# Optimization experiments

Measured on AMD Instinct MI355X. Metric: run time of the kernel, lower is better.

The kernel has to match this reference:

```python
import jax, jax.numpy as jnp
import numpy as np

INPUT_SIZE = 256
HIDDEN_SIZE = 512
OUTPUT_SIZE = 256
SEQ_LEN = 32768


def setup_inputs() -> dict:
    key = jax.random.key(0)
    k_x, k_wx, k_wh, k_wy = jax.random.split(key, 4)
    x = jax.random.normal(k_x, (SEQ_LEN, INPUT_SIZE), dtype=jnp.float32)
    Wx = jax.random.normal(k_wx, (HIDDEN_SIZE, INPUT_SIZE), dtype=jnp.float32) * np.sqrt(2.0 / (INPUT_SIZE + HIDDEN_SIZE))
    Wh = jax.random.normal(k_wh, (HIDDEN_SIZE, HIDDEN_SIZE), dtype=jnp.float32) * np.sqrt(1.0 / HIDDEN_SIZE)
    Wy = jax.random.normal(k_wy, (OUTPUT_SIZE, HIDDEN_SIZE), dtype=jnp.float32) * np.sqrt(2.0 / (HIDDEN_SIZE + OUTPUT_SIZE))
    bh = jnp.zeros((HIDDEN_SIZE, 1), dtype=jnp.float32)
    by = jnp.zeros((OUTPUT_SIZE, 1), dtype=jnp.float32)
    return {"x": x, "Wx": Wx, "Wh": Wh, "Wy": Wy, "bh": bh, "by": by}


def reference(x, Wx, Wh, Wy, bh, by):
    # x: [T, I]; Wx: [H, I]; Wh: [H, H]; Wy: [O, H]; bh: [H,1]; by: [O,1]
    bh_v = bh[:, 0]  # [H]
    by_v = by[:, 0]  # [O]
    h0 = jnp.zeros((Wh.shape[0],), dtype=x.dtype)

    def step(h, x_t):
        # h_t = tanh(Wx @ x_t + Wh @ h_{t-1} + bh)
        h_new = jnp.tanh(Wx @ x_t + Wh @ h + bh_v)
        return h_new, h_new

    _, h_hist = jax.lax.scan(step, h0, x)  # [T, H]
    # y_t = Wy @ h_t + by, concatenated and flattened -> [T * O]
    y = h_hist @ Wy.T + by_v  # [T, O]
    return y.reshape(-1)
```

## Files before the change

### kernel.cpp

```cpp
#include <hip/hip_runtime.h>

#define SEQ 32768
#define ISZ 256
#define HSZ 512
#define OSZ 256
#define NLAUNCH 64
#define RTHREADS 576
#define SENT 0x7FAAAAAAu
#define KFAST 8
#define LATCH_T 48

typedef unsigned long long u64;
typedef _Float16 half2_t __attribute__((ext_vector_type(2)));

#if defined(__has_builtin)
#if __has_builtin(__builtin_amdgcn_fdot2)
#define HAVE_FDOT2 1
#endif
#endif

__device__ __forceinline__ float dot2f(half2_t a, half2_t b, float c) {
#ifdef HAVE_FDOT2
  return __builtin_amdgcn_fdot2(a, b, c, false);
#else
  return fmaf((float)a.x, (float)b.x, fmaf((float)a.y, (float)b.y, c));
#endif
}
__device__ __forceinline__ half2_t bch2(unsigned u) {
  return __builtin_bit_cast(half2_t, u);
}
__device__ __forceinline__ unsigned pkrtz_u(float x, float y) {
  return __builtin_bit_cast(unsigned, __builtin_amdgcn_cvt_pkrtz(x, y));
}

__global__ __launch_bounds__(256) void gemm_bt_bias(
    const float* __restrict__ A, const float* __restrict__ W,
    const float* __restrict__ bias, float* __restrict__ C,
    int M, int N, int K)
{
  __shared__ float As[32][68];
  __shared__ float Bs[32][68];
  const int tx = threadIdx.x;
  const int tn = tx & 15, tm = tx >> 4;
  const int m0 = blockIdx.x * 64, n0 = blockIdx.y * 64;
  const int kl = tx & 31;
  const int rl = tx >> 5;
  float acc[4][4] = {};

  for (int kt = 0; kt < K; kt += 32) {
#pragma unroll
    for (int i = 0; i < 8; ++i) {
      int m = rl + i * 8;
      As[kl][m] = A[(size_t)(m0 + m) * K + kt + kl];
      Bs[kl][m] = W[(size_t)(n0 + m) * K + kt + kl];
    }
    __syncthreads();
#pragma unroll
    for (int k = 0; k < 32; ++k) {
      float a[4], b[4];
#pragma unroll
      for (int i = 0; i < 4; ++i) a[i] = As[k][tm * 4 + i];
#pragma unroll
      for (int j = 0; j < 4; ++j) b[j] = Bs[k][tn * 4 + j];
#pragma unroll
      for (int i = 0; i < 4; ++i)
#pragma unroll
        for (int j = 0; j < 4; ++j)
          acc[i][j] = fmaf(a[i], b[j], acc[i][j]);
    }
    __syncthreads();
  }
#pragma unroll
  for (int i = 0; i < 4; ++i) {
    int m = m0 + tm * 4 + i;
#pragma unroll
    for (int j = 0; j < 4; ++j) {
      int n = n0 + tn * 4 + j;
      C[(size_t)m * N + n] = acc[i][j] + bias[n];
    }
  }
}

__device__ __forceinline__ float poll_sent(const float* p, unsigned sent) {
  float a, b;
  asm volatile(
      "s_waitcnt vmcnt(0)\n\t"
      "global_load_dword %0, %2, off sc0 sc1\n\t"
      "global_load_dword %1, %2, off sc0 sc1\n"
      "1:\n\t"
      "s_waitcnt vmcnt(1)\n\t"
      "v_cmp_eq_u32 vcc, %3, %0\n\t"
      "s_cbranch_vccz 3f\n\t"
      "global_load_dword %0, %2, off sc0 sc1\n\t"
      "s_waitcnt vmcnt(1)\n\t"
      "v_cmp_eq_u32 vcc, %3, %1\n\t"
      "s_cbranch_vccz 2f\n\t"
      "global_load_dword %1, %2, off sc0 sc1\n\t"
      "s_branch 1b\n"
      "2:\n\t"
      "v_mov_b32 %0, %1\n"
      "3:\n\t"
      "s_waitcnt vmcnt(0)"
      : "=&v"(a), "=&v"(b)
      : "v"(p), "v"(sent)
      : "memory", "vcc");
  return a;
}

__device__ __forceinline__ u64 load_fast(const u64* p) {
  u64 v;
  asm volatile("global_load_dwordx2 %0, %1, off sc0\n\t"
               "s_waitcnt vmcnt(0)"
               : "=v"(v) : "v"(p) : "memory");
  return v;
}
__device__ __forceinline__ void store_fast(u64* p, u64 v) {
  asm volatile("global_store_dwordx2 %0, %1, off sc0" :: "v"(p), "v"(v)
               : "memory");
}

__global__ __launch_bounds__(RTHREADS, 2) void rnn_recur(
    const float* __restrict__ P,
    const float* __restrict__ Wh,
    float* __restrict__ h_hist,
    u64* __restrict__ fring)
{
  const int b = blockIdx.x;
  if (b & 7) return;
  const int g = b >> 3;
  const int tid = threadIdx.x;
  const int w = tid >> 6;
  const int l = tid & 63;
  const int g64 = g << 6;

  __shared__ float part[2][8][64];
  __shared__ float hown[2][64];
  __shared__ int   wflag[8];
  __shared__ int   hofl;
  if (tid < 8) wflag[tid] = 0;
  if (tid == 8) hofl = 0;
  __syncthreads();

  if (w == 8) {
    float pv = P[g64 + l];
    for (int t = 0; t < SEQ; ++t) {
      const int buf = t & 1;
      int fv;
      do {
        fv = __hip_atomic_load(&wflag[l & 7], __ATOMIC_ACQUIRE,
                               __HIP_MEMORY_SCOPE_WORKGROUP);
      } while (__any((int)(fv < t + 1)));
      float s = 0.f;
#pragma unroll
      for (int q = 0; q < 8; ++q) s += part[buf][q][l];
      float xv = s + pv;
      xv = fminf(fmaxf(xv, -15.f), 15.f);
      float e = __expf(2.f * xv);
      float hn = 1.f - 2.f / (e + 1.f);
      __hip_atomic_store(&h_hist[(size_t)(t + 1) * HSZ + g64 + l], hn,
                         __ATOMIC_RELAXED, __HIP_MEMORY_SCOPE_AGENT);
      const u64 pk = ((u64)(unsigned)(t + 1) << 32) | (u64)__float_as_uint(hn);
      const int slot = (t + 1) & 3;
#pragma unroll
      for (int j = 0; j < 8; ++j)
        store_fast(fring + (((size_t)j * 4 + slot) * 8 + g) * 64 + l, pk);
      hown[(t + 1) & 1][l] = hn;
      if (l == 0)
        __hip_atomic_store(&hofl, t + 1, __ATOMIC_RELEASE,
                           __HIP_MEMORY_SCOPE_WORKGROUP);
      pv = P[(size_t)(t + 1 < SEQ ? t + 1 : SEQ - 1) * HSZ + g64 + l];
    }
    return;
  }

  const int row = g64 + l;
  const int kbase = w << 6;

  unsigned wreg[32];
  {
    const float2* ws = (const float2*)(Wh + (size_t)row * HSZ + kbase);
#pragma unroll
    for (int j = 0; j < 32; ++j) {
      float2 f = ws[j];
      unsigned u = pkrtz_u(f.x, f.y);
      asm("" : "+v"(u));
      wreg[j] = u;
    }
  }

  const bool lds_path = (w == g);
  int fastok = 0;
  int use_fast = 1;

  for (int t = 0; t < SEQ; ++t) {
    float vh = 0.f;
    if (t > 0) {
      if (lds_path) {
        while (__hip_atomic_load(&hofl, __ATOMIC_ACQUIRE,
                                 __HIP_MEMORY_SCOPE_WORKGROUP) < t) { }
        vh = hown[t & 1][l];
      } else {
        int got = 0;
        if (use_fast) {
          const u64* fp = fring + (((size_t)g * 4 + (t & 3)) * 8 + w) * 64 + l;
          for (int k = 0; k < KFAST; ++k) {
            u64 v = load_fast(fp);
            if (__all((int)((unsigned)(v >> 32) == (unsigned)t))) {
              vh = __uint_as_float((unsigned)v);
              got = 1;
              break;
            }
          }
          if (t <= LATCH_T) {
            fastok += got;
            if (t == LATCH_T && fastok < LATCH_T - 8) use_fast = 0;
          }
        }
        if (!got)
          vh = poll_sent(h_hist + (size_t)t * HSZ + kbase + l, SENT);
      }
    }

    float vn = __shfl_xor(vh, 1);
    unsigned hpu = pkrtz_u(vh, vn);
    float a0 = 0.f, a1 = 0.f, a2 = 0.f, a3 = 0.f;
#pragma unroll
    for (int j = 0; j < 8; ++j) {
      a0 = dot2f(bch2(wreg[4 * j + 0]),
                 bch2(__builtin_amdgcn_readlane(hpu, 8 * j + 0)), a0);
      a1 = dot2f(bch2(wreg[4 * j + 1]),
                 bch2(__builtin_amdgcn_readlane(hpu, 8 * j + 2)), a1);
      a2 = dot2f(bch2(wreg[4 * j + 2]),
                 bch2(__builtin_amdgcn_readlane(hpu, 8 * j + 4)), a2);
      a3 = dot2f(bch2(wreg[4 * j + 3]),
                 bch2(__builtin_amdgcn_readlane(hpu, 8 * j + 6)), a3);
    }
    part[t & 1][w][l] = (a0 + a1) + (a2 + a3);
    if (l == 0)
      __hip_atomic_store(&wflag[w], t + 1, __ATOMIC_RELEASE,
                         __HIP_MEMORY_SCOPE_WORKGROUP);
  }
}

extern "C" void kernel_launch(void* const* d_in, const int* in_sizes, int n_in,
                              void* d_out, int out_size, void* d_ws, size_t ws_size,
                              hipStream_t stream) {
  const float* x  = (const float*)d_in[0];
  const float* Wx = (const float*)d_in[1];
  const float* Wh = (const float*)d_in[2];
  const float* Wy = (const float*)d_in[3];
  const float* bh = (const float*)d_in[4];
  const float* by = (const float*)d_in[5];
  float* out = (float*)d_out;

  float* P      = (float*)d_ws;
  float* h_hist = P + (size_t)SEQ * HSZ;
  u64*   fring  = (u64*)(h_hist + (size_t)(SEQ + 1) * HSZ);

  (void)hipMemsetD32Async((hipDeviceptr_t)h_hist, (int)SENT,
                          (size_t)(SEQ + 1) * HSZ, stream);
  (void)hipMemsetAsync(h_hist, 0, HSZ * sizeof(float), stream);
  (void)hipMemsetAsync(fring, 0, (size_t)8 * 4 * 8 * 64 * sizeof(u64), stream);

  gemm_bt_bias<<<dim3(SEQ / 64, HSZ / 64), dim3(256), 0, stream>>>(
      x, Wx, bh, P, SEQ, HSZ, ISZ);

  rnn_recur<<<dim3(NLAUNCH), dim3(RTHREADS), 0, stream>>>(P, Wh, h_hist, fring);

  gemm_bt_bias<<<dim3(SEQ / 64, OSZ / 64), dim3(256), 0, stream>>>(
      h_hist + HSZ, Wy, by, out, SEQ, OSZ, HSZ);
}
```

Measured before the change: 32.00 ms.

## Co-locate recurrence blocks on one XCC and fold reducer into home wave

Blocks now elect roles at runtime by reading the XCC id, so the eight working recurrence blocks all sit on the same chiplet and cross-block hidden-state exchange stays inside one L2. The separate reducer wave and its LDS flag handshakes are removed. A __syncthreads now follows the partial-sum write, and the home wave performs the reduction and tanh itself, keeping its own h in a register. This targets the per-step cross-XCC latency and the flag polling, at the cost of a full block barrier every step and a dependence on the block scheduler placing at least eight blocks on one XCC.

```diff
diff --git a/kernel.cpp b/kernel.cpp
--- a/kernel.cpp
+++ b/kernel.cpp
@@ -5,7 +5,7 @@
 #define HSZ 512
 #define OSZ 256
 #define NLAUNCH 64
-#define RTHREADS 576
+#define RTHREADS 512
 #define SENT 0x7FAAAAAAu
 #define KFAST 8
 #define LATCH_T 48
@@ -123,56 +123,44 @@
     const float* __restrict__ P,
     const float* __restrict__ Wh,
     float* __restrict__ h_hist,
-    u64* __restrict__ fring)
+    u64* __restrict__ fring,
+    int* __restrict__ elect)
 {
-  const int b = blockIdx.x;
-  if (b & 7) return;
-  const int g = b >> 3;
   const int tid = threadIdx.x;
   const int w = tid >> 6;
   const int l = tid & 63;
+
+  __shared__ float part[2][8][64];
+  __shared__ int s_role;
+
+  if (tid == 0) {
+    unsigned xcc;
+    asm volatile("s_getreg_b32 %0, hwreg(HW_REG_XCC_ID)" : "=s"(xcc));
+    xcc &= 7u;
+    int role = -1;
+    int r = __hip_atomic_fetch_add(&elect[xcc], 1, __ATOMIC_RELAXED,
+                                   __HIP_MEMORY_SCOPE_AGENT);
+    if (r < 8) {
+      if (r == 7) {
+        int exp_ = -1;
+        (void)__hip_atomic_compare_exchange_strong(
+            &elect[8], &exp_, (int)xcc,
+            __ATOMIC_RELEASE, __ATOMIC_RELAXED, __HIP_MEMORY_SCOPE_AGENT);
+      }
+      int wv;
+      do {
+        wv = __hip_atomic_load(&elect[8], __ATOMIC_ACQUIRE,
+                               __HIP_MEMORY_SCOPE_AGENT);
+      } while (wv < 0);
+      if (wv == (int)xcc) role = r;
+    }
+    s_role = role;
+  }
+  __syncthreads();
+  const int g = s_role;
+  if (g < 0) return;
+
   const int g64 = g << 6;
-
-  __shared__ float part[2][8][64];
-  __shared__ float hown[2][64];
-  __shared__ int   wflag[8];
-  __shared__ int   hofl;
-  if (tid < 8) wflag[tid] = 0;
-  if (tid == 8) hofl = 0;
-  __syncthreads();
-
-  if (w == 8) {
-    float pv = P[g64 + l];
-    for (int t = 0; t < SEQ; ++t) {
-      const int buf = t & 1;
-      int fv;
-      do {
-        fv = __hip_atomic_load(&wflag[l & 7], __ATOMIC_ACQUIRE,
-                               __HIP_MEMORY_SCOPE_WORKGROUP);
-      } while (__any((int)(fv < t + 1)));
-      float s = 0.f;
-#pragma unroll
-      for (int q = 0; q < 8; ++q) s += part[buf][q][l];
-      float xv = s + pv;
-      xv = fminf(fmaxf(xv, -15.f), 15.f);
-      float e = __expf(2.f * xv);
-      float hn = 1.f - 2.f / (e + 1.f);
-      __hip_atomic_store(&h_hist[(size_t)(t + 1) * HSZ + g64 + l], hn,
-                         __ATOMIC_RELAXED, __HIP_MEMORY_SCOPE_AGENT);
-      const u64 pk = ((u64)(unsigned)(t + 1) << 32) | (u64)__float_as_uint(hn);
-      const int slot = (t + 1) & 3;
-#pragma unroll
-      for (int j = 0; j < 8; ++j)
-        store_fast(fring + (((size_t)j * 4 + slot) * 8 + g) * 64 + l, pk);
-      hown[(t + 1) & 1][l] = hn;
-      if (l == 0)
-        __hip_atomic_store(&hofl, t + 1, __ATOMIC_RELEASE,
-                           __HIP_MEMORY_SCOPE_WORKGROUP);
-      pv = P[(size_t)(t + 1 < SEQ ? t + 1 : SEQ - 1) * HSZ + g64 + l];
-    }
-    return;
-  }
-
   const int row = g64 + l;
   const int kbase = w << 6;
 
@@ -188,37 +176,35 @@
     }
   }
 
-  const bool lds_path = (w == g);
-  int fastok = 0;
-  int use_fast = 1;
+  const bool home = (w == g);
+  float hreg = 0.f;
+  float pv = home ? P[row] : 0.f;
+  float pvn = 0.f;
+  int fastok = 0, use_fast = 1;
 
   for (int t = 0; t < SEQ; ++t) {
     float vh = 0.f;
-    if (t > 0) {
-      if (lds_path) {
-        while (__hip_atomic_load(&hofl, __ATOMIC_ACQUIRE,
-                                 __HIP_MEMORY_SCOPE_WORKGROUP) < t) { }
-        vh = hown[t & 1][l];
-      } else {
-        int got = 0;
-        if (use_fast) {
-          const u64* fp = fring + (((size_t)g * 4 + (t & 3)) * 8 + w) * 64 + l;
-          for (int k = 0; k < KFAST; ++k) {
-            u64 v = load_fast(fp);
-            if (__all((int)((unsigned)(v >> 32) == (unsigned)t))) {
-              vh = __uint_as_float((unsigned)v);
-              got = 1;
-              break;
-            }
-          }
-          if (t <= LATCH_T) {
-            fastok += got;
-            if (t == LATCH_T && fastok < LATCH_T - 8) use_fast = 0;
+    if (home) {
+      vh = hreg;
+    } else if (t > 0) {
+      int got = 0;
+      if (use_fast) {
+        const u64* fp = fring + (((size_t)g * 4 + (t & 3)) * 8 + w) * 64 + l;
+        for (int k = 0; k < KFAST; ++k) {
+          u64 v = load_fast(fp);
+          if (__all((int)((unsigned)(v >> 32) == (unsigned)t))) {
+            vh = __uint_as_float((unsigned)v);
+            got = 1;
+            break;
           }
         }
-        if (!got)
-          vh = poll_sent(h_hist + (size_t)t * HSZ + kbase + l, SENT);
+        if (t <= LATCH_T) {
+          fastok += got;
+          if (t == LATCH_T && fastok < LATCH_T - 8) use_fast = 0;
+        }
       }
+      if (!got)
+        vh = poll_sent(h_hist + (size_t)t * HSZ + kbase + l, SENT);
     }
 
     float vn = __shfl_xor(vh, 1);
@@ -236,9 +222,31 @@
                  bch2(__builtin_amdgcn_readlane(hpu, 8 * j + 6)), a3);
     }
     part[t & 1][w][l] = (a0 + a1) + (a2 + a3);
-    if (l == 0)
-      __hip_atomic_store(&wflag[w], t + 1, __ATOMIC_RELEASE,
-                         __HIP_MEMORY_SCOPE_WORKGROUP);
+
+    __syncthreads();
+
+    if (home) {
+      pvn = P[(size_t)(t + 1 < SEQ ? t + 1 : SEQ - 1) * HSZ + row];
+      const int buf = t & 1;
+      float p0 = part[buf][0][l], p1 = part[buf][1][l];
+      float p2 = part[buf][2][l], p3 = part[buf][3][l];
+      float p4 = part[buf][4][l], p5 = part[buf][5][l];
+      float p6 = part[buf][6][l], p7 = part[buf][7][l];
+      float s = ((p0 + p1) + (p2 + p3)) + ((p4 + p5) + (p6 + p7));
+      float xv = s + pv;
+      xv = fminf(fmaxf(xv, -15.f), 15.f);
+      float e = __expf(2.f * xv);
+      float hn = fmaf(-2.f, __builtin_amdgcn_rcpf(e + 1.f), 1.f);
+      hreg = hn;
+      const u64 pk = ((u64)(unsigned)(t + 1) << 32) | (u64)__float_as_uint(hn);
+      const int slot = (t + 1) & 3;
+#pragma unroll
+      for (int j = 0; j < 8; ++j)
+        store_fast(fring + (((size_t)j * 4 + slot) * 8 + g) * 64 + l, pk);
+      __hip_atomic_store(&h_hist[(size_t)(t + 1) * HSZ + row], hn,
+                         __ATOMIC_RELAXED, __HIP_MEMORY_SCOPE_AGENT);
+      pv = pvn;
+    }
   }
 }
 
@@ -256,16 +264,20 @@
   float* P      = (float*)d_ws;
   float* h_hist = P + (size_t)SEQ * HSZ;
   u64*   fring  = (u64*)(h_hist + (size_t)(SEQ + 1) * HSZ);
+  int*   elect  = (int*)(fring + (size_t)8 * 4 * 8 * 64);
 
   (void)hipMemsetD32Async((hipDeviceptr_t)h_hist, (int)SENT,
                           (size_t)(SEQ + 1) * HSZ, stream);
   (void)hipMemsetAsync(h_hist, 0, HSZ * sizeof(float), stream);
   (void)hipMemsetAsync(fring, 0, (size_t)8 * 4 * 8 * 64 * sizeof(u64), stream);
+  (void)hipMemsetAsync(elect, 0, 8 * sizeof(int), stream);
+  (void)hipMemsetAsync(elect + 8, 0xFF, sizeof(int), stream);
 
   gemm_bt_bias<<<dim3(SEQ / 64, HSZ / 64), dim3(256), 0, stream>>>(
       x, Wx, bh, P, SEQ, HSZ, ISZ);
 
-  rnn_recur<<<dim3(NLAUNCH), dim3(RTHREADS), 0, stream>>>(P, Wh, h_hist, fring);
+  rnn_recur<<<dim3(NLAUNCH), dim3(RTHREADS), 0, stream>>>(
+      P, Wh, h_hist, fring, elect);
 
   gemm_bt_bias<<<dim3(SEQ / 64, OSZ / 64), dim3(256), 0, stream>>>(
       h_hist + HSZ, Wy, by, out, SEQ, OSZ, HSZ);
```

New measurement: 29.30 ms. -8.4%, faster.
